# Kernel tuning notes

Hardware: AMD Instinct MI355X
Metric: run time of the kernel (lower is better)

Reference implementation:

```python
import jax, jax.numpy as jnp
import numpy as np
import math

B, T, C, H = 4, 2048, 1024, 16

def setup_inputs() -> dict:
    key = jax.random.key(0)
    ks = jax.random.split(key, 7)
    s = 0.02
    return {
        'x':  jax.random.normal(ks[0], (B, T, C), dtype=jnp.float32),
        'Wq': jax.random.normal(ks[1], (C, C), dtype=jnp.float32) * s,
        'bq': jnp.zeros((C,), dtype=jnp.float32),
        'Wk': jax.random.normal(ks[2], (C, C), dtype=jnp.float32) * s,
        'bk': jnp.zeros((C,), dtype=jnp.float32),
        'Wv': jax.random.normal(ks[3], (C, C), dtype=jnp.float32) * s,
        'bv': jnp.zeros((C,), dtype=jnp.float32),
    }

def reference(x, Wq, bq, Wk, bk, Wv, bv):
    # Dropouts are identity (eval mode). Note: the original module reuses
    # v_proj as the output projection -- reproduced faithfully.
    b, t, c = x.shape
    hs = c // H
    q = (x @ Wq + bq).reshape(b, t, H, hs).transpose(0, 2, 1, 3)  # [B,H,T,hs]
    k = (x @ Wk + bk).reshape(b, t, H, hs).transpose(0, 2, 1, 3)
    v = (x @ Wv + bv).reshape(b, t, H, hs).transpose(0, 2, 1, 3)
    att = jnp.einsum('bhqd,bhkd->bhqk', q, k) * (1.0 / math.sqrt(hs))
    causal = jnp.tril(jnp.ones((t, t), dtype=bool))
    att = jnp.where(causal[None, None], att, -jnp.inf)
    att = jax.nn.softmax(att, axis=-1)
    y = jnp.einsum('bhqk,bhkd->bhqd', att, v)  # [B,H,T,hs]
    y = y.transpose(0, 2, 1, 3).reshape(b, t, c)
    y = y @ Wv + bv  # module applies v_proj again as output projection
    return y
```

## Files before the change

kernel.cpp:

```cpp
#include <hip/hip_runtime.h>
#include <hip/hip_bf16.h>

typedef __bf16 bf16;
typedef __attribute__((ext_vector_type(8))) __bf16 bf16x8;
typedef __attribute__((ext_vector_type(4))) __bf16 bf16x4;
typedef __attribute__((ext_vector_type(2))) __bf16 bf16x2;
typedef __attribute__((ext_vector_type(4))) float f32x4;
typedef __attribute__((ext_vector_type(2))) unsigned int u32x2;
typedef __attribute__((ext_vector_type(4))) unsigned int u32x4;

#define MFMA16(a, b, c) __builtin_amdgcn_mfma_f32_16x16x32_bf16((a), (b), (c), 0, 0, 0)
#define SM_SCALE 0.18033688011112043f

__device__ __forceinline__ void gld_lds16(const bf16* g, bf16* l) {
    __builtin_amdgcn_global_load_lds((const __attribute__((address_space(1))) void*)g,
                                     (__attribute__((address_space(3))) void*)l, 16, 0, 0);
}

#define PBAR() asm volatile("s_barrier" ::: "memory")
#define VWAIT0() asm volatile("s_waitcnt vmcnt(0)" ::: "memory")
#define VWAIT3() asm volatile("s_waitcnt vmcnt(3)" ::: "memory")
#define VWAIT4() asm volatile("s_waitcnt vmcnt(4)" ::: "memory")

__global__ __launch_bounds__(256) void prep(const float* __restrict__ W0,
                                            const float* __restrict__ W1,
                                            const float* __restrict__ W2,
                                            bf16* __restrict__ Wt,
                                            const float* __restrict__ xin,
                                            bf16* __restrict__ xout) {
    __shared__ float tile[64][65];
    const int blk = blockIdx.x;
    const int tid = threadIdx.x;
    if (blk < 768) {
        const int z = blk >> 8, rem = blk & 255;
        const int r0 = (rem >> 4) * 64;
        const int c0 = (rem & 15) * 64;
        const float* W = (z == 0) ? W0 : ((z == 1) ? W1 : W2);
        bf16* dst = Wt + (size_t)z * 1024 * 1024;
        for (int i = tid; i < 4096; i += 256) {
            int r = i >> 6, cc = i & 63;
            tile[r][cc] = W[(size_t)(r0 + r) * 1024 + c0 + cc];
        }
        __syncthreads();
        for (int i = tid; i < 4096; i += 256) {
            int n = i >> 6, k = i & 63;
            dst[(size_t)(c0 + n) * 1024 + r0 + k] = (bf16)tile[k][n];
        }
    } else {
        const size_t i0 = ((size_t)(blk - 768) * 256 + tid) * 16;
#pragma unroll
        for (int j = 0; j < 2; j++) {
            const float4 v0 = *(const float4*)(xin + i0 + j * 8);
            const float4 v1 = *(const float4*)(xin + i0 + j * 8 + 4);
            bf16x8 o = {(bf16)v0.x, (bf16)v0.y, (bf16)v0.z, (bf16)v0.w,
                        (bf16)v1.x, (bf16)v1.y, (bf16)v1.z, (bf16)v1.w};
            *(bf16x8*)(xout + i0 + j * 8) = o;
        }
    }
}

template <int MODE>
__global__ __launch_bounds__(512, 4) void gemm_main(const bf16* __restrict__ A,
                                                    const bf16* __restrict__ Bt,
                                                    const float* __restrict__ b0,
                                                    const float* __restrict__ b1,
                                                    const float* __restrict__ b2,
                                                    void* __restrict__ out0,
                                                    void* __restrict__ out1,
                                                    void* __restrict__ out2,
                                                    int nbx) {
    __shared__ alignas(16) bf16 LDS[3 * 12288];

    const int orig = blockIdx.x;
    const int chunk = (int)gridDim.x >> 3;
    const int swz = (orig & 7) * chunk + (orig >> 3);
    const int by = swz / nbx, bx = swz % nbx;
    const int m0 = by * 256, n0 = bx * 128;

    const int tid = threadIdx.x;
    const int wid = tid >> 6, lane = tid & 63;
    const int wr = wid >> 1, wc = wid & 1;
    const int quad = lane >> 4, l16 = lane & 15;

    const int sr = tid >> 2;
    const int scol = (((tid & 3) ^ ((sr >> 1) & 3)) * 8);
    const bf16* gA = A + (size_t)(m0 + sr) * 1024 + scol;
    const bf16* gB = Bt + (size_t)(n0 + sr) * 1024 + scol;
    bf16* lA = &LDS[tid * 8];
    bf16* lB = &LDS[8192 + tid * 8];

    const int coff = ((quad ^ ((l16 >> 1) & 3)) * 8);

    f32x4 acc[4][4] = {};

    auto STAGE = [&](int kt, int p) {
        const int base = p * 12288;
        gld_lds16(gA + kt * 32, lA + base);
        gld_lds16(gA + kt * 32 + (size_t)128 * 1024, lA + base + 4096);
        gld_lds16(gB + kt * 32, lB + base);
    };

    STAGE(0, 0);
    STAGE(1, 1);
    VWAIT3();
    PBAR();

    int rb = 0;
    int sb = 2;
#pragma unroll 1
    for (int kt = 0; kt < 32; kt++) {
        const bf16* Asp = &LDS[rb * 12288];
        const bf16* Bsp = Asp + 8192;
        if (kt + 2 < 32) STAGE(kt + 2, sb);

        bf16x8 af[4], bfr[4];
#pragma unroll
        for (int m4 = 0; m4 < 4; m4++)
            af[m4] = *(const bf16x8*)&Asp[(wr * 64 + m4 * 16 + l16) * 32 + coff];
#pragma unroll
        for (int ni = 0; ni < 4; ni++)
            bfr[ni] = *(const bf16x8*)&Bsp[(wc * 64 + ni * 16 + l16) * 32 + coff];

        __builtin_amdgcn_s_setprio(1);
#pragma unroll
        for (int m4 = 0; m4 < 4; m4++)
#pragma unroll
            for (int ni = 0; ni < 4; ni++)
                acc[m4][ni] = MFMA16(af[m4], bfr[ni], acc[m4][ni]);
        __builtin_amdgcn_s_setprio(0);

        if (kt < 30) {
            VWAIT3();
            PBAR();
        } else if (kt == 30) {
            VWAIT0();
            PBAR();
        }
        rb = (rb == 2) ? 0 : rb + 1;
        sb = (sb == 2) ? 0 : sb + 1;
    }

    const int nl0 = (n0 & 1023) + wc * 64;
    const int mb0 = m0 + wr * 64;
    if (MODE == 0) {
        const int sel = n0 >> 10;
        if (sel < 2) {
            const float* bias = (sel == 0) ? b0 : b1;
            bf16* Cp = (bf16*)((sel == 0) ? out0 : out1);
            const float qs = (sel == 0) ? SM_SCALE : 1.0f;
#pragma unroll
            for (int mi = 0; mi < 4; mi++) {
                const int mbase = mb0 + mi * 16 + quad * 4;
#pragma unroll
                for (int ni = 0; ni < 4; ni++) {
                    const int nl = nl0 + ni * 16 + l16;
                    const float bv = bias[nl];
#pragma unroll
                    for (int r = 0; r < 4; r++)
                        Cp[(size_t)(mbase + r) * 1024 + nl] =
                            (bf16)((acc[mi][ni][r] + bv) * qs);
                }
            }
        } else {
            bf16* Vt = (bf16*)out2;
            const int b = m0 >> 11;
#pragma unroll
            for (int ni = 0; ni < 4; ni++) {
                const int nl = nl0 + ni * 16 + l16;
                const int h = nl >> 6, d = nl & 63;
                const float bv = b2[nl];
                bf16* dst = Vt + ((size_t)(b * 16 + h) * 64 + d) * 2048;
#pragma unroll
                for (int mi = 0; mi < 4; mi++) {
                    const int t0 = (mb0 + mi * 16 + quad * 4) & 2047;
                    bf16x4 w = {(bf16)(acc[mi][ni][0] + bv), (bf16)(acc[mi][ni][1] + bv),
                                (bf16)(acc[mi][ni][2] + bv), (bf16)(acc[mi][ni][3] + bv)};
                    *(bf16x4*)&dst[t0] = w;
                }
            }
        }
    } else {
        float* Cp = (float*)out0;
#pragma unroll
        for (int mi = 0; mi < 4; mi++) {
            const int mbase = mb0 + mi * 16 + quad * 4;
#pragma unroll
            for (int ni = 0; ni < 4; ni++) {
                const int n = n0 + wc * 64 + ni * 16 + l16;
                const float bv = b0[n];
#pragma unroll
                for (int r = 0; r < 4; r++)
                    Cp[(size_t)(mbase + r) * 1024 + n] = acc[mi][ni][r] + bv;
            }
        }
    }
}

template <bool NEEDMASK>
__device__ __forceinline__ void softmax_reg(const f32x4* st, bf16x8* pf, int qrel) {
    unsigned int p[4][2];
#pragma unroll
    for (int j = 0; j < 4; j++) {
        float pv[4];
#pragma unroll
        for (int r = 0; r < 4; r++) {
            float s = st[j][r];
            if (NEEDMASK && (j * 16 + r > qrel)) s = -1e30f;
            pv[r] = __builtin_amdgcn_exp2f(s);
        }
        bf16x2 w0 = {(bf16)pv[0], (bf16)pv[1]};
        bf16x2 w1 = {(bf16)pv[2], (bf16)pv[3]};
        p[j][0] = __builtin_bit_cast(unsigned int, w0);
        p[j][1] = __builtin_bit_cast(unsigned int, w1);
    }
#pragma unroll
    for (int ks = 0; ks < 2; ks++) {
        unsigned int q4[4];
#pragma unroll
        for (int h = 0; h < 2; h++) {
            u32x2 s32 = __builtin_amdgcn_permlane32_swap(p[2 * ks][h], p[2 * ks + 1][h],
                                                         false, false);
            u32x2 s16 = __builtin_amdgcn_permlane16_swap(s32[0], s32[1], false, false);
            q4[h] = s16[0];
            q4[2 + h] = s16[1];
        }
        u32x4 qq = {q4[0], q4[1], q4[2], q4[3]};
        pf[ks] = __builtin_bit_cast(bf16x8, qq);
    }
}

__global__ __launch_bounds__(256, 2) void attn(const bf16* __restrict__ Q,
                                               const bf16* __restrict__ Kg,
                                               const bf16* __restrict__ Vt,
                                               bf16* __restrict__ O) {
    const int lin = blockIdx.x;
    const int bh = (lin & 7) * 8 + ((lin >> 3) & 7);
    const int jb = lin >> 6;
    const int b = bh >> 4, h = bh & 15;
    const int tid = threadIdx.x;
    const int wave = tid >> 6, lane = tid & 63;
    const int quad = lane >> 4, l16 = lane & 15;

    __shared__ alignas(16) bf16 KVs[3 * 8192];

    const bf16* Kbase = Kg + ((size_t)b * 2048) * 1024 + h * 64;
    const bf16* Vbase = Vt + (size_t)bh * 64 * 2048;

    const int srow = tid >> 3;
    const int schunk = (tid & 7) ^ (srow & 7);

    const int xorE = (l16 & 7) * 8;
    const int cofA = (quad * 8) ^ xorE;
    const int cofB = (32 + quad * 8) ^ xorE;

    const bf16 one1 = (bf16)1.0f;
    const bf16x8 onesf = {one1, one1, one1, one1, one1, one1, one1, one1};

#pragma unroll 1
    for (int phase = 0; phase < 2; phase++) {
        const int js = (phase == 0) ? (15 - jb) : jb;
        const int q0 = js * 128;
        const bf16* Qbase = Q + ((size_t)(b * 2048 + q0)) * 1024 + h * 64;

        bf16x8 qfA[2], qfB[2];
#pragma unroll
        for (int ks = 0; ks < 2; ks++) {
            qfA[ks] = *(const bf16x8*)&Qbase[(size_t)(wave * 16 + l16) * 1024 + ks * 32 + quad * 8];
            qfB[ks] = *(const bf16x8*)&Qbase[(size_t)(64 + wave * 16 + l16) * 1024 + ks * 32 + quad * 8];
        }

        f32x4 otA[4] = {}, otB[4] = {};
        f32x4 laccA = {0.f, 0.f, 0.f, 0.f}, laccB = {0.f, 0.f, 0.f, 0.f};
        const int ntiles = 2 * js + 2;
        const int qrel = wave * 16 + l16 - quad * 4;

        const bf16* pK = Kbase + (size_t)srow * 1024 + schunk * 8;
        const bf16* pK2 = pK + (size_t)32 * 1024;
        const bf16* pV = Vbase + (size_t)srow * 2048 + schunk * 8;
        const bf16* pV2 = pV + (size_t)32 * 2048;

        {
            bf16* nb = &KVs[tid * 8];
            gld_lds16(pK, nb);
            gld_lds16(pK2, nb + 2048);
            gld_lds16(pV, nb + 4096);
            gld_lds16(pV2, nb + 6144);
            pK += 64 * 1024; pK2 += 64 * 1024; pV += 64; pV2 += 64;
            nb = &KVs[8192 + tid * 8];
            gld_lds16(pK, nb);
            gld_lds16(pK2, nb + 2048);
            gld_lds16(pV, nb + 4096);
            gld_lds16(pV2, nb + 6144);
            pK += 64 * 1024; pK2 += 64 * 1024; pV += 64; pV2 += 64;
        }
        VWAIT4();
        PBAR();

        int rbuf = 0, sbuf = 2;
#pragma unroll 1
        for (int tk = 0; tk < ntiles; tk++) {
            const bf16* buf = &KVs[rbuf * 8192];
            if (tk + 2 < ntiles) {
                bf16* nb = &KVs[sbuf * 8192 + tid * 8];
                gld_lds16(pK, nb);
                gld_lds16(pK2, nb + 2048);
                gld_lds16(pV, nb + 4096);
                gld_lds16(pV2, nb + 6144);
                pK += 64 * 1024; pK2 += 64 * 1024; pV += 64; pV2 += 64;
            }

            f32x4 stA[4] = {}, stB[4] = {};
#pragma unroll
            for (int ks = 0; ks < 2; ks++)
#pragma unroll
                for (int j = 0; j < 4; j++) {
                    const bf16x8 kf =
                        *(const bf16x8*)&buf[(j * 16 + l16) * 64 + (ks ? cofB : cofA)];
                    stA[j] = MFMA16(kf, qfA[ks], stA[j]);
                    stB[j] = MFMA16(kf, qfB[ks], stB[j]);
                }

            bf16x8 pfA[2], pfB[2];
            if (tk < ntiles - 2) {
                softmax_reg<false>(stA, pfA, qrel);
                softmax_reg<false>(stB, pfB, qrel);
            } else if (tk == ntiles - 2) {
                softmax_reg<true>(stA, pfA, qrel);
                softmax_reg<false>(stB, pfB, qrel);
            } else {
                softmax_reg<true>(stA, pfA, qrel - 64);
                softmax_reg<true>(stB, pfB, qrel);
            }

            laccA = MFMA16(onesf, pfA[0], laccA);
            laccA = MFMA16(onesf, pfA[1], laccA);
            laccB = MFMA16(onesf, pfB[0], laccB);
            laccB = MFMA16(onesf, pfB[1], laccB);

#pragma unroll
            for (int ks = 0; ks < 2; ks++)
#pragma unroll
                for (int db = 0; db < 4; db++) {
                    const bf16x8 vf = *(const bf16x8*)&buf[4096 + (db * 16 + l16) * 64 +
                                                           (ks ? cofB : cofA)];
                    otA[db] = MFMA16(vf, pfA[ks], otA[db]);
                    otB[db] = MFMA16(vf, pfB[ks], otB[db]);
                }

            if (tk + 1 < ntiles) {
                if (tk + 2 < ntiles) VWAIT4();
                else VWAIT0();
                PBAR();
            }
            rbuf = (rbuf == 2) ? 0 : rbuf + 1;
            sbuf = (sbuf == 2) ? 0 : sbuf + 1;
        }

        bf16* ep = &KVs[((ntiles + 1) % 3) * 8192 + wave * (16 * 72)];
        const int orow = lane >> 2, oc = (lane & 3) * 16;
        {
            const float inv = 1.f / laccA[0];
#pragma unroll
            for (int db = 0; db < 4; db++) {
                bf16x4 w = {(bf16)(otA[db][0] * inv), (bf16)(otA[db][1] * inv),
                            (bf16)(otA[db][2] * inv), (bf16)(otA[db][3] * inv)};
                *(bf16x4*)&ep[l16 * 72 + db * 16 + quad * 4] = w;
            }
            bf16* Obase =
                O + ((size_t)(b * 2048 + q0 + wave * 16 + orow)) * 1024 + h * 64 + oc;
            const bf16* src = &ep[orow * 72 + oc];
            *(bf16x8*)&Obase[0] = *(const bf16x8*)&src[0];
            *(bf16x8*)&Obase[8] = *(const bf16x8*)&src[8];
        }
        {
            const float inv = 1.f / laccB[0];
#pragma unroll
            for (int db = 0; db < 4; db++) {
                bf16x4 w = {(bf16)(otB[db][0] * inv), (bf16)(otB[db][1] * inv),
                            (bf16)(otB[db][2] * inv), (bf16)(otB[db][3] * inv)};
                *(bf16x4*)&ep[l16 * 72 + db * 16 + quad * 4] = w;
            }
            bf16* Obase =
                O + ((size_t)(b * 2048 + q0 + 64 + wave * 16 + orow)) * 1024 + h * 64 + oc;
            const bf16* src = &ep[orow * 72 + oc];
            *(bf16x8*)&Obase[0] = *(const bf16x8*)&src[0];
            *(bf16x8*)&Obase[8] = *(const bf16x8*)&src[8];
        }
        __syncthreads();
    }
}

extern "C" void kernel_launch(void* const* d_in, const int* in_sizes, int n_in,
                              void* d_out, int out_size, void* d_ws, size_t ws_size,
                              hipStream_t stream) {
    const float* x = (const float*)d_in[0];
    const float* Wq = (const float*)d_in[1];
    const float* bq = (const float*)d_in[2];
    const float* Wk = (const float*)d_in[3];
    const float* bk = (const float*)d_in[4];
    const float* Wv = (const float*)d_in[5];
    const float* bv = (const float*)d_in[6];
    float* out = (float*)d_out;

    const int M = 8192;
    const size_t sz_x = (size_t)M * 1024;
    const size_t sz_w = (size_t)1024 * 1024;

    char* p = (char*)d_ws;
    bf16* xb = (bf16*)p;   p += sz_x * 2;
    bf16* Wcat = (bf16*)p; p += 3 * sz_w * 2;
    bf16* qb = (bf16*)p;   p += sz_x * 2;
    bf16* kb = (bf16*)p;   p += sz_x * 2;
    bf16* Vt = (bf16*)p;   p += sz_x * 2;
    bf16* yatt = (bf16*)p; p += sz_x * 2;

    prep<<<dim3(2816), dim3(256), 0, stream>>>(Wq, Wk, Wv, Wcat, x, xb);

    gemm_main<0><<<dim3(768), dim3(512), 0, stream>>>(xb, Wcat, bq, bk, bv, qb, kb, Vt, 24);
    attn<<<dim3(512), dim3(256), 0, stream>>>(qb, kb, Vt, yatt);
    gemm_main<1><<<dim3(256), dim3(512), 0, stream>>>(yatt, Wcat + 2 * sz_w, bv, bv, bv,
                                                      out, out, out, 8);
}
```

Baseline: 228.1 us.

## Split QKV GEMM into dedicated kernel with 256x192 tiles and 12 waves

```diff
diff --git a/kernel.cpp b/kernel.cpp
--- a/kernel.cpp
+++ b/kernel.cpp
@@ -19,6 +19,7 @@
 
 #define PBAR() asm volatile("s_barrier" ::: "memory")
 #define VWAIT0() asm volatile("s_waitcnt vmcnt(0)" ::: "memory")
+#define VWAIT2() asm volatile("s_waitcnt vmcnt(2)" ::: "memory")
 #define VWAIT3() asm volatile("s_waitcnt vmcnt(3)" ::: "memory")
 #define VWAIT4() asm volatile("s_waitcnt vmcnt(4)" ::: "memory")
 
@@ -59,15 +60,123 @@
     }
 }
 
-template <int MODE>
-__global__ __launch_bounds__(512, 4) void gemm_main(const bf16* __restrict__ A,
+__global__ __launch_bounds__(768, 3) void gemm_qkv(const bf16* __restrict__ A,
+                                                   const bf16* __restrict__ Bt,
+                                                   const float* __restrict__ b0,
+                                                   const float* __restrict__ b1,
+                                                   const float* __restrict__ b2,
+                                                   bf16* __restrict__ qb,
+                                                   bf16* __restrict__ kb,
+                                                   bf16* __restrict__ Vt) {
+    __shared__ alignas(16) bf16 LDS[3 * 14336];
+
+    const int orig = blockIdx.x;
+    const int swz = (orig & 7) * 64 + (orig >> 3);
+    const int by = swz >> 4, bx = swz & 15;
+    const int m0 = by * 256, n0 = bx * 192;
+
+    const int tid = threadIdx.x;
+    const int wid = tid >> 6, lane = tid & 63;
+    const int wr = wid / 3, wcn = wid % 3;
+    const int quad = lane >> 4, l16 = lane & 15;
+
+    const bool bstage = (wid < 4);
+    const int schunk = (lane & 3) ^ ((lane >> 3) & 3);
+    const int srow0 = (bstage ? wid * 48 : (wid - 4) * 32) + (lane >> 2);
+    const bf16* gsrc = (bstage ? Bt + (size_t)(n0 + srow0) * 1024
+                               : A + (size_t)(m0 + srow0) * 1024) + schunk * 8;
+    const int ldst0 = (bstage ? 8192 + wid * 1536 : (wid - 4) * 1024) + lane * 8;
+
+    const int coff = ((quad ^ ((l16 >> 1) & 3)) * 8);
+
+    f32x4 acc[4][4] = {};
+
+    auto STAGE = [&](int kt, int p) {
+        bf16* d = &LDS[p * 14336 + ldst0];
+        const bf16* s = gsrc + kt * 32;
+        gld_lds16(s, d);
+        gld_lds16(s + (size_t)16 * 1024, d + 512);
+        if (bstage) gld_lds16(s + (size_t)32 * 1024, d + 1024);
+    };
+
+    STAGE(0, 0);
+    STAGE(1, 1);
+    if (bstage) VWAIT3(); else VWAIT2();
+    PBAR();
+
+    int rb = 0;
+    int sb = 2;
+#pragma unroll 1
+    for (int kt = 0; kt < 32; kt++) {
+        const bf16* Asp = &LDS[rb * 14336];
+        const bf16* Bsp = Asp + 8192;
+        if (kt + 2 < 32) STAGE(kt + 2, sb);
+
+        bf16x8 af[4], bfr[4];
+#pragma unroll
+        for (int m4 = 0; m4 < 4; m4++)
+            af[m4] = *(const bf16x8*)&Asp[(wr * 64 + m4 * 16 + l16) * 32 + coff];
+#pragma unroll
+        for (int ni = 0; ni < 4; ni++)
+            bfr[ni] = *(const bf16x8*)&Bsp[(wcn * 64 + ni * 16 + l16) * 32 + coff];
+
+        __builtin_amdgcn_s_setprio(1);
+#pragma unroll
+        for (int m4 = 0; m4 < 4; m4++)
+#pragma unroll
+            for (int ni = 0; ni < 4; ni++)
+                acc[m4][ni] = MFMA16(af[m4], bfr[ni], acc[m4][ni]);
+        __builtin_amdgcn_s_setprio(0);
+
+        if (kt < 30) {
+            if (bstage) VWAIT3(); else VWAIT2();
+            PBAR();
+        } else if (kt == 30) {
+            VWAIT0();
+            PBAR();
+        }
+        rb = (rb == 2) ? 0 : rb + 1;
+        sb = (sb == 2) ? 0 : sb + 1;
+    }
+
+    const int mb0 = m0 + wr * 64;
+#pragma unroll
+    for (int ni = 0; ni < 4; ni++) {
+        const int nlg = n0 + wcn * 64 + ni * 16 + l16;
+        const int sel = nlg >> 10;
+        const int nl = nlg & 1023;
+        if (sel < 2) {
+            const float* bias = sel ? b1 : b0;
+            bf16* Cp = sel ? kb : qb;
+            const float qs = sel ? 1.0f : SM_SCALE;
+            const float bv = bias[nl];
+#pragma unroll
+            for (int mi = 0; mi < 4; mi++) {
+                const int mbase = mb0 + mi * 16 + quad * 4;
+#pragma unroll
+                for (int r = 0; r < 4; r++)
+                    Cp[(size_t)(mbase + r) * 1024 + nl] = (bf16)((acc[mi][ni][r] + bv) * qs);
+            }
+        } else {
+            const int h = nl >> 6, d = nl & 63;
+            const float bv = b2[nl];
+            const int bb = m0 >> 11;
+            bf16* dst = Vt + ((size_t)(bb * 16 + h) * 64 + d) * 2048;
+#pragma unroll
+            for (int mi = 0; mi < 4; mi++) {
+                const int t0 = (mb0 + mi * 16 + quad * 4) & 2047;
+                bf16x4 w = {(bf16)(acc[mi][ni][0] + bv), (bf16)(acc[mi][ni][1] + bv),
+                            (bf16)(acc[mi][ni][2] + bv), (bf16)(acc[mi][ni][3] + bv)};
+                *(bf16x4*)&dst[t0] = w;
+            }
+        }
+    }
+}
+
+__global__ __launch_bounds__(512, 4) void gemm_proj(const bf16* __restrict__ A,
                                                     const bf16* __restrict__ Bt,
                                                     const float* __restrict__ b0,
-                                                    const float* __restrict__ b1,
-                                                    const float* __restrict__ b2,
-                                                    void* __restrict__ out0,
-                                                    void* __restrict__ out1,
-                                                    void* __restrict__ out2,
+                                                    float* __restrict__ out0,
                                                     int nbx) {
     __shared__ alignas(16) bf16 LDS[3 * 12288];
 
@@ -105,8 +214,7 @@
     VWAIT3();
     PBAR();
 
-    int rb = 0;
-    int sb = 2;
+    int rb = 0, sb = 2;
 #pragma unroll 1
     for (int kt = 0; kt < 32; kt++) {
         const bf16* Asp = &LDS[rb * 12288];
@@ -140,58 +248,17 @@
         sb = (sb == 2) ? 0 : sb + 1;
     }
 
-    const int nl0 = (n0 & 1023) + wc * 64;
     const int mb0 = m0 + wr * 64;
-    if (MODE == 0) {
-        const int sel = n0 >> 10;
-        if (sel < 2) {
-            const float* bias = (sel == 0) ? b0 : b1;
-            bf16* Cp = (bf16*)((sel == 0) ? out0 : out1);
-            const float qs = (sel == 0) ? SM_SCALE : 1.0f;
-#pragma unroll
-            for (int mi = 0; mi < 4; mi++) {
-                const int mbase = mb0 + mi * 16 + quad * 4;
-#pragma unroll
-                for (int ni = 0; ni < 4; ni++) {
-                    const int nl = nl0 + ni * 16 + l16;
-                    const float bv = bias[nl];
-#pragma unroll
-                    for (int r = 0; r < 4; r++)
-                        Cp[(size_t)(mbase + r) * 1024 + nl] =
-                            (bf16)((acc[mi][ni][r] + bv) * qs);
-                }
-            }
-        } else {
-            bf16* Vt = (bf16*)out2;
-            const int b = m0 >> 11;
-#pragma unroll
-            for (int ni = 0; ni < 4; ni++) {
-                const int nl = nl0 + ni * 16 + l16;
-                const int h = nl >> 6, d = nl & 63;
-                const float bv = b2[nl];
-                bf16* dst = Vt + ((size_t)(b * 16 + h) * 64 + d) * 2048;
-#pragma unroll
-                for (int mi = 0; mi < 4; mi++) {
-                    const int t0 = (mb0 + mi * 16 + quad * 4) & 2047;
-                    bf16x4 w = {(bf16)(acc[mi][ni][0] + bv), (bf16)(acc[mi][ni][1] + bv),
-                                (bf16)(acc[mi][ni][2] + bv), (bf16)(acc[mi][ni][3] + bv)};
-                    *(bf16x4*)&dst[t0] = w;
-                }
-            }
-        }
-    } else {
-        float* Cp = (float*)out0;
-#pragma unroll
-        for (int mi = 0; mi < 4; mi++) {
-            const int mbase = mb0 + mi * 16 + quad * 4;
-#pragma unroll
-            for (int ni = 0; ni < 4; ni++) {
-                const int n = n0 + wc * 64 + ni * 16 + l16;
-                const float bv = b0[n];
-#pragma unroll
-                for (int r = 0; r < 4; r++)
-                    Cp[(size_t)(mbase + r) * 1024 + n] = acc[mi][ni][r] + bv;
-            }
+#pragma unroll
+    for (int mi = 0; mi < 4; mi++) {
+        const int mbase = mb0 + mi * 16 + quad * 4;
+#pragma unroll
+        for (int ni = 0; ni < 4; ni++) {
+            const int n = n0 + wc * 64 + ni * 16 + l16;
+            const float bv = b0[n];
+#pragma unroll
+            for (int r = 0; r < 4; r++)
+                out0[(size_t)(mbase + r) * 1024 + n] = acc[mi][ni][r] + bv;
         }
     }
 }
@@ -416,8 +483,7 @@
 
     prep<<<dim3(2816), dim3(256), 0, stream>>>(Wq, Wk, Wv, Wcat, x, xb);
 
-    gemm_main<0><<<dim3(768), dim3(512), 0, stream>>>(xb, Wcat, bq, bk, bv, qb, kb, Vt, 24);
+    gemm_qkv<<<dim3(512), dim3(768), 0, stream>>>(xb, Wcat, bq, bk, bv, qb, kb, Vt);
     attn<<<dim3(512), dim3(256), 0, stream>>>(qb, kb, Vt, yatt);
-    gemm_main<1><<<dim3(256), dim3(512), 0, stream>>>(yatt, Wcat + 2 * sz_w, bv, bv, bv,
-                                                      out, out, out, 8);
-}
+    gemm_proj<<<dim3(256), dim3(512), 0, stream>>>(yatt, Wcat + 2 * sz_w, bv, out, 8);
+}
```

Result: no change. 230.7 us (+1.1%).
